# Optimization experiments

Hardware: AMD Instinct MI355X
Metric: run time of the kernel (lower is better)

Reference implementation:

```python
import jax, jax.numpy as jnp
import numpy as np

B, V, L, C, CA = 4, 16, 1024, 256, 256
MASK_VAL = 1e10  # original: triu(ones) * 10**10 subtracted pre-softmax


def setup_inputs() -> dict:
    key = jax.random.key(0)
    ks = jax.random.split(key, 10)
    s = 0.05  # keep logits in a sane range; math is init-independent
    return {
        "X": jax.random.normal(ks[0], (B, V, L, C), jnp.float32),
        "Qw": jax.random.normal(ks[1], (V, C, CA), jnp.float32) * s,
        "Kw": jax.random.normal(ks[2], (V, C, CA), jnp.float32) * s,
        "Vw": jax.random.normal(ks[3], (V, C, CA), jnp.float32) * s,
        "Qb": jax.random.normal(ks[4], (CA,), jnp.float32) * s,
        "Kb": jax.random.normal(ks[5], (CA,), jnp.float32) * s,
        "Vb": jax.random.normal(ks[6], (CA,), jnp.float32) * s,
        "gama": jax.random.normal(ks[7], (1,), jnp.float32),
        "fc_w": jax.random.normal(ks[8], (C, CA), jnp.float32) * s,
        "fc_b": jax.random.normal(ks[9], (C,), jnp.float32) * s,
    }


def reference(X, Qw, Kw, Vw, Qb, Kb, Vb, gama, fc_w, fc_b):
    # per-variable projections: [B,v,L,C] x [v,C,Ca] -> [B,v,L,Ca]
    Q = jnp.einsum('bvlc,vca->bvla', X, Qw) + Qb
    K = jnp.einsum('bvlc,vca->bvla', X, Kw) + Kb
    Vp = jnp.einsum('bvlc,vca->bvla', X, Vw) + Vb
    # causal mask subtraction (no 1/sqrt(d) scaling in the original)
    Lc = X.shape[2]
    mask = jnp.triu(jnp.ones((Lc, Lc), X.dtype), 1) * MASK_VAL
    scores = jnp.einsum('bvla,bvma->bvlm', Q, K) - mask  # [B,v,L,L]
    alpha = jax.nn.softmax(scores, axis=-1)
    Va = jnp.einsum('bvlm,bvma->bvla', alpha, Vp)        # [B,v,L,Ca]
    # gated fc + residual: X + gama * fc(Va)
    return X + (jnp.einsum('bvla,ca->bvlc', Va, fc_w) + fc_b) * gama
```

## Files before the change

kernel.cpp:

```cpp
#include <hip/hip_runtime.h>

typedef __bf16 bf16_8 __attribute__((ext_vector_type(8)));
typedef float f32x4 __attribute__((ext_vector_type(4)));

#define MFMA16(a, b, c) __builtin_amdgcn_mfma_f32_16x16x32_bf16(a, b, c, 0, 0, 0)


__device__ __forceinline__ void load_lds16(const char* g, char* l) {
  __builtin_amdgcn_global_load_lds(
      (const __attribute__((address_space(1))) unsigned int*)g,
      (__attribute__((address_space(3))) unsigned int*)l, 16, 0, 0);
}

__global__ __launch_bounds__(256) void prep_kernel(
    const float* __restrict__ Qw, const float* __restrict__ Kw,
    const float* __restrict__ Vw, const float* __restrict__ fcw,
    const float* __restrict__ X,
    __bf16* __restrict__ Wfq, __bf16* __restrict__ Wfk,
    __bf16* __restrict__ Wfv, __bf16* __restrict__ fcb,
    __bf16* __restrict__ Xb)
{
  const int bid = blockIdx.x, t = threadIdx.x;
  if (bid < 192) {
    __shared__ __bf16 lds[64][264];
    const int m = bid >> 2, cblk = bid & 3;
    const int wsel = m >> 4, v = m & 15;
    const float* src = (wsel == 0 ? Qw : wsel == 1 ? Kw : Vw) + (size_t)v * 65536;
    __bf16* dst = (wsel == 0 ? Wfq : wsel == 1 ? Wfk : Wfv) + (size_t)v * 65536;
    const int c0 = cblk * 64;
    const int cl = t >> 2, seg = t & 3;
#pragma unroll
    for (int i = 0; i < 16; ++i) {
      float4 f = *(const float4*)(src + (size_t)(c0 + cl) * 256 + seg * 64 + i * 4);
      lds[cl][seg * 64 + i * 4 + 0] = (__bf16)f.x;
      lds[cl][seg * 64 + i * 4 + 1] = (__bf16)f.y;
      lds[cl][seg * 64 + i * 4 + 2] = (__bf16)f.z;
      lds[cl][seg * 64 + i * 4 + 3] = (__bf16)f.w;
    }
    __syncthreads();
    const int nn = t >> 4, l16 = t & 15;
#pragma unroll
    for (int i = 0; i < 8; ++i) {
      bf16_8 vv;
#pragma unroll
      for (int j = 0; j < 8; ++j) vv[j] = lds[i * 8 + j][t];
      const int c = c0 + i * 8;
      const int ks = c >> 5, lg = (c & 31) >> 3;
      const int g = (ks * 16 + nn) * 64 + lg * 16 + l16;
      *(bf16_8*)(dst + (size_t)g * 8) = vv;
    }
  } else if (bid < 208) {
    const int g0 = (bid - 192) * 512 + t * 2;
#pragma unroll
    for (int h = 0; h < 2; ++h) {
      int g = g0 + h;
      int ks = g >> 10, n = (g >> 6) & 15, lane = g & 63;
      const float* src = fcw + (size_t)(n * 16 + (lane & 15)) * 256
                             + ks * 32 + (lane >> 4) * 8;
      float4 f0 = *(const float4*)(src);
      float4 f1 = *(const float4*)(src + 4);
      bf16_8 vv;
      vv[0] = (__bf16)f0.x; vv[1] = (__bf16)f0.y; vv[2] = (__bf16)f0.z; vv[3] = (__bf16)f0.w;
      vv[4] = (__bf16)f1.x; vv[5] = (__bf16)f1.y; vv[6] = (__bf16)f1.z; vv[7] = (__bf16)f1.w;
      *(bf16_8*)(fcb + (size_t)g * 8) = vv;
    }
  } else {
    const size_t base = (size_t)(bid - 208) * 8192 + t * 32;
#pragma unroll
    for (int h = 0; h < 4; ++h) {
      float4 f0 = *(const float4*)(X + base + h * 8);
      float4 f1 = *(const float4*)(X + base + h * 8 + 4);
      bf16_8 vv;
      vv[0] = (__bf16)f0.x; vv[1] = (__bf16)f0.y; vv[2] = (__bf16)f0.z; vv[3] = (__bf16)f0.w;
      vv[4] = (__bf16)f1.x; vv[5] = (__bf16)f1.y; vv[6] = (__bf16)f1.z; vv[7] = (__bf16)f1.w;
      *(bf16_8*)(Xb + base + h * 8) = vv;
    }
  }
}

__global__ __launch_bounds__(256, 2) void proj_kernel(
    const __bf16* __restrict__ Xb,
    const __bf16* __restrict__ Wfq, const __bf16* __restrict__ Wfk,
    const __bf16* __restrict__ Wfv,
    const float* __restrict__ Qb, const float* __restrict__ Kb,
    const float* __restrict__ Vb,
    __bf16* __restrict__ Qo, __bf16* __restrict__ Ko, __bf16* __restrict__ VTo,
    int bv0)
{
  extern __shared__ char psmem[];
  char* rpb = psmem + 65536;

  const int t = threadIdx.x;
  const int w = t >> 6, lane = t & 63;
  const int l16 = lane & 15, lg = lane >> 4;

  const int nwg = gridDim.x * gridDim.y;
  const int hw = blockIdx.x + gridDim.x * blockIdx.y;
  int bvl, r12;
  if (nwg % 96 == 0) {
    const int per = nwg >> 3;
    const int lid = (hw & 7) * per + (hw >> 3);
    bvl = lid / 12; r12 = lid - bvl * 12;
  } else { bvl = blockIdx.y; r12 = blockIdx.x; }
  const int z = r12 >> 2, nh = (r12 >> 1) & 1, rh = r12 & 1;
  const int bvg = bv0 + bvl, v = bvg & 15;

  const __bf16* Wf = (z == 0 ? Wfq : z == 1 ? Wfk : Wfv) + (size_t)v * 65536;
  const float* bias = (z == 0 ? Qb : z == 1 ? Kb : Vb) + nh * 128;

  bf16_8 bw0[8], bw1[8];
#pragma unroll
  for (int ks = 0; ks < 8; ++ks) {
    const int nnb = nh * 8 + w * 2;
    bw0[ks] = *(const bf16_8*)(Wf + ((size_t)(ks * 16 + nnb) * 64 + lane) * 8);
    bw1[ks] = *(const bf16_8*)(Wf + ((size_t)(ks * 16 + nnb + 1) * 64 + lane) * 8);
  }

  const char* xb = (const char*)(Xb + ((size_t)(bvg * 1024 + rh * 512)) * 256);
  auto stageX = [&](int it, int pb) {
    const char* src0 = xb + (size_t)it * 32768;
    char* dst0 = psmem + pb * 32768;
#pragma unroll
    for (int i = 0; i < 8; ++i) {
      int p = i * 256 + t, r = p >> 5, c16 = p & 31;
      load_lds16(src0 + r * 512 + ((c16 * 16) ^ ((r & 7) << 4)),
                 dst0 + (i * 256 + w * 64) * 16);
    }
  };

  stageX(0, 0);

  const float bn0 = bias[w * 32 + l16];
  const float bn1 = bias[w * 32 + 16 + l16];
  f32x4 zero = {0.f, 0.f, 0.f, 0.f};
  const int xsw = (l16 & 7) << 4;

  for (int it = 0; it < 8; ++it) {
    const int cur = it & 1;
    __builtin_amdgcn_s_barrier();
    if (it < 7) {
      stageX(it + 1, cur ^ 1);
      asm volatile("s_waitcnt vmcnt(8)" ::: "memory");
    } else {
      asm volatile("s_waitcnt vmcnt(0)" ::: "memory");
    }
    __builtin_amdgcn_s_barrier();

    f32x4 acc[4][2];
#pragma unroll
    for (int m = 0; m < 4; ++m) { acc[m][0] = zero; acc[m][1] = zero; }

    const char* xt = psmem + cur * 32768 + l16 * 512;
#pragma unroll
    for (int ks = 0; ks < 8; ++ks) {
      const int co = (ks * 64 + lg * 16) ^ xsw;
      bf16_8 af[4];
#pragma unroll
      for (int m = 0; m < 4; ++m)
        af[m] = *(const bf16_8*)(xt + m * 8192 + co);
#pragma unroll
      for (int m = 0; m < 4; ++m) {
        acc[m][0] = MFMA16(af[m], bw0[ks], acc[m][0]);
        acc[m][1] = MFMA16(af[m], bw1[ks], acc[m][1]);
      }
    }

    const int row0 = rh * 512 + it * 64;
#pragma unroll
    for (int n = 0; n < 2; ++n) {
      float bn = n ? bn1 : bn0;
      int col2 = (w * 32 + n * 16 + l16) * 2;
#pragma unroll
      for (int m = 0; m < 4; ++m)
#pragma unroll
        for (int j = 0; j < 4; ++j) {
          int r = m * 16 + lg * 4 + j;
          *(__bf16*)(rpb + r * 256 + (col2 ^ ((r & 7) << 4))) = (__bf16)(acc[m][n][j] + bn);
        }
    }
    asm volatile("s_waitcnt lgkmcnt(0)" ::: "memory");
    __builtin_amdgcn_s_barrier();

    if (z < 2) {
      __bf16* out = (z == 0 ? Qo : Ko) + (size_t)(bvl * 1024 + row0) * 256;
#pragma unroll
      for (int i = 0; i < 4; ++i) {
        int e = i * 256 + t, rr = e >> 4, cl = (e & 15) * 8;
        bf16_8 d = *(const bf16_8*)(rpb + rr * 256 + ((cl * 2) ^ ((rr & 7) << 4)));
        int gcol = (z == 1) ? (nh * 128 + (cl ^ ((rr & 7) * 8))) : (nh * 128 + cl);
        *(bf16_8*)(out + (size_t)rr * 256 + gcol) = d;
      }
    } else {
      const int kt = rh * 8 + it;
      const int cal = t >> 1, half = t & 1;
      __bf16* dst = VTo + (size_t)bvl * 262144 + (size_t)kt * 16384
                    + (size_t)(nh * 128 + cal) * 64;
#pragma unroll
      for (int i = 0; i < 4; ++i) {
        int q = half * 4 + i;
        int k0 = (q ^ (cal & 7)) * 8;
        bf16_8 vv;
#pragma unroll
        for (int j = 0; j < 8; ++j)
          vv[j] = *(const __bf16*)(rpb + (k0 + j) * 256 + ((cal * 2) ^ (j << 4)));
        *(bf16_8*)(dst + q * 8) = vv;
      }
    }
  }
}

__global__ __launch_bounds__(512, 2) void attn_kernel(
    const __bf16* __restrict__ Qg, const __bf16* __restrict__ Kg,
    const __bf16* __restrict__ VTg, const __bf16* __restrict__ Fc,
    const float* __restrict__ Xg, const float* __restrict__ fc_b,
    const float* __restrict__ gama, float* __restrict__ Out, int bv0)
{
  extern __shared__ char smem[];
  __bf16 (*Pt)[72] = (__bf16(*)[72])(smem + 131072);

  const int t = threadIdx.x;
  const int w = t >> 6, lane = t & 63;
  const int l16 = lane & 15, lg = lane >> 4;

  const int nwg = gridDim.x * gridDim.y;
  const int hw = blockIdx.x + gridDim.x * blockIdx.y;
  int bvl, qb;
  if (nwg == 512) {
    const int x = hw & 7, j = hw >> 3;
    bvl = x * 8 + ((j >> 5) << 2) + (j & 3);
    qb  = 7 - ((j >> 2) & 7);
  } else { bvl = blockIdx.x; qb = 7 - (int)blockIdx.y; }
  const int bvg = bv0 + bvl;
  const int ktmax = 2 * qb + 1;

  const char* Kb = (const char*)(Kg + (size_t)bvl * 262144);
  const char* Vb = (const char*)(VTg + (size_t)bvl * 262144);

  bf16_8 qf[8];
  const __bf16* qp = Qg + ((size_t)(bvl * 1024 + qb * 128 + w * 16 + l16)) * 256 + lg * 8;
#pragma unroll
  for (int ks = 0; ks < 8; ++ks) qf[ks] = *(const bf16_8*)(qp + ks * 32);

  f32x4 zero = {0.f, 0.f, 0.f, 0.f};
  f32x4 oacc[16];
#pragma unroll
  for (int n = 0; n < 16; ++n) oacc[n] = zero;
  float rs[4] = {0.f, 0.f, 0.f, 0.f};

  const int swz = (l16 & 7) << 4;
  const int p1 = (lg * 16) ^ (swz & 0x30);
  const int o_e = swz & 0x40;
  const int o_o = 64 ^ (swz & 0x40);

  auto stage = [&](int kt, int pb) {
    const char* kg = Kb + (size_t)kt * 32768;
    const char* vg = Vb + (size_t)kt * 32768;
    char* kl = smem + pb * 32768;
    char* vl = smem + 65536 + pb * 32768;
#pragma unroll
    for (int i = 0; i < 4; ++i) {
      int go = (i * 512 + t) * 16;
      int lo = (i * 512 + w * 64) * 16;
      load_lds16(kg + go, kl + lo);
      load_lds16(vg + go, vl + lo);
    }
  };

  stage(0, 0);

  for (int kt = 0; kt <= ktmax; ++kt) {
    const int cur = kt & 1;

    __builtin_amdgcn_s_barrier();
    if (kt < ktmax) {
      stage(kt + 1, cur ^ 1);
      asm volatile("s_waitcnt vmcnt(8)" ::: "memory");
    } else {
      asm volatile("s_waitcnt vmcnt(0)" ::: "memory");
    }
    __builtin_amdgcn_s_barrier();

    const bool skip = (kt * 64) > (qb * 128 + w * 16 + 15);
    if (!skip) {
      const char* krow = smem + cur * 32768 + l16 * 512 + p1;
      f32x4 sacc[4];
#pragma unroll
      for (int n = 0; n < 4; ++n) sacc[n] = zero;
      __builtin_amdgcn_s_setprio(1);
#pragma unroll
      for (int ks = 0; ks < 8; ++ks) {
        const int cb = (ks >> 1) * 128 + ((ks & 1) ? o_o : o_e);
#pragma unroll
        for (int n = 0; n < 4; ++n) {
          bf16_8 kb = *(const bf16_8*)(krow + n * 8192 + cb);
          sacc[n] = MFMA16(qf[ks], kb, sacc[n]);
        }
      }
      __builtin_amdgcn_s_setprio(0);

      const bool edge = (kt * 64 + 63) > (qb * 128 + w * 16);
      const int qrow = qb * 128 + w * 16 + lg * 4;
#pragma unroll
      for (int n = 0; n < 4; ++n) {
        int kglob = kt * 64 + n * 16 + l16;
#pragma unroll
        for (int j = 0; j < 4; ++j) {
          float p = __expf(sacc[n][j]);
          if (edge && kglob > qrow + j) p = 0.f;
          rs[j] += p;
          Pt[w * 16 + lg * 4 + j][n * 16 + l16] = (__bf16)p;
        }
      }
      asm volatile("s_waitcnt lgkmcnt(0)" ::: "memory");

      const char* vrow = smem + 65536 + cur * 32768 + l16 * 128 + p1;
      __builtin_amdgcn_s_setprio(1);
#pragma unroll
      for (int k2 = 0; k2 < 2; ++k2) {
        bf16_8 pa = *(const bf16_8*)&Pt[w * 16 + l16][k2 * 32 + lg * 8];
        const int cb = k2 ? o_o : o_e;
#pragma unroll
        for (int n = 0; n < 16; ++n) {
          bf16_8 vv = *(const bf16_8*)(vrow + n * 2048 + cb);
          oacc[n] = MFMA16(pa, vv, oacc[n]);
        }
      }
      __builtin_amdgcn_s_setprio(0);
    }
  }

  __syncthreads();

#pragma unroll
  for (int j = 0; j < 4; ++j) {
    float s = rs[j];
    s += __shfl_xor(s, 1); s += __shfl_xor(s, 2);
    s += __shfl_xor(s, 4); s += __shfl_xor(s, 8);
    rs[j] = 1.0f / s;
  }

  __bf16* Va = (__bf16*)smem;
#pragma unroll
  for (int n = 0; n < 16; ++n) {
#pragma unroll
    for (int j = 0; j < 4; ++j) {
      int r = w * 16 + lg * 4 + j;
      int c = n * 16 + l16;
      Va[r * 256 + (c ^ ((r & 7) * 8))] = (__bf16)(oacc[n][j] * rs[j]);
    }
  }
  __syncthreads();

  f32x4 facc[16];
#pragma unroll
  for (int n = 0; n < 16; ++n) facc[n] = zero;
#pragma unroll
  for (int ks = 0; ks < 8; ++ks) {
    int cc = (ks * 32 + lg * 8) ^ ((l16 & 7) * 8);
    bf16_8 pa = *(const bf16_8*)(Va + (w * 16 + l16) * 256 + cc);
    const __bf16* fp = Fc + (size_t)ks * 8192 + lane * 8;
#pragma unroll
    for (int n = 0; n < 16; ++n) {
      bf16_8 fb = *(const bf16_8*)(fp + n * 512);
      facc[n] = MFMA16(pa, fb, facc[n]);
    }
  }

  const float g = gama[0];
  const size_t base = ((size_t)(bvg * 1024 + qb * 128 + w * 16)) * 256;
#pragma unroll
  for (int n = 0; n < 16; ++n) {
    int col = n * 16 + l16;
    float fbc = fc_b[col];
#pragma unroll
    for (int j = 0; j < 4; ++j) {
      size_t idx = base + (size_t)(lg * 4 + j) * 256 + col;
      Out[idx] = Xg[idx] + (facc[n][j] + fbc) * g;
    }
  }
}

extern "C" void kernel_launch(void* const* d_in, const int* in_sizes, int n_in,
                              void* d_out, int out_size, void* d_ws, size_t ws_size,
                              hipStream_t stream) {
  const float* X    = (const float*)d_in[0];
  const float* Qw   = (const float*)d_in[1];
  const float* Kw   = (const float*)d_in[2];
  const float* Vw   = (const float*)d_in[3];
  const float* Qb   = (const float*)d_in[4];
  const float* Kb   = (const float*)d_in[5];
  const float* Vb   = (const float*)d_in[6];
  const float* gama = (const float*)d_in[7];
  const float* fcw  = (const float*)d_in[8];
  const float* fcb  = (const float*)d_in[9];
  float* out = (float*)d_out;

  char* ws = (char*)d_ws;
  const size_t wbytes = (size_t)(6u << 20) + (128u << 10) + (32u << 20);
  const size_t perbv  = 3ull * 1024 * 256 * 2;
  if (ws_size < wbytes + perbv) return;
  int chunk = (int)((ws_size - wbytes) / perbv);
  if (chunk > 64) chunk = 64;
  int nchunks = (64 + chunk - 1) / chunk;
  chunk = (64 + nchunks - 1) / nchunks;

  __bf16* Wfq = (__bf16*)(ws);
  __bf16* Wfk = (__bf16*)(ws + (2u << 20));
  __bf16* Wfv = (__bf16*)(ws + (4u << 20));
  __bf16* Fcb = (__bf16*)(ws + (6u << 20));
  __bf16* Xb  = (__bf16*)(ws + (6u << 20) + (128u << 10));
  __bf16* Qo  = (__bf16*)(ws + wbytes);
  __bf16* Ko  = Qo + (size_t)chunk * 262144;
  __bf16* VTo = Ko + (size_t)chunk * 262144;

  prep_kernel<<<2256, 256, 0, stream>>>(Qw, Kw, Vw, fcw, X, Wfq, Wfk, Wfv, Fcb, Xb);

  const int psmem = 2 * 32768 + 64 * 128 * 2;
  (void)hipFuncSetAttribute(reinterpret_cast<const void*>(proj_kernel),
                            hipFuncAttributeMaxDynamicSharedMemorySize, psmem);
  const int smem = 4 * 32768 + 128 * 72 * 2;
  (void)hipFuncSetAttribute(reinterpret_cast<const void*>(attn_kernel),
                            hipFuncAttributeMaxDynamicSharedMemorySize, smem);

  for (int bv0 = 0; bv0 < 64; bv0 += chunk) {
    int nb = 64 - bv0; if (nb > chunk) nb = chunk;
    proj_kernel<<<dim3(12, nb), 256, psmem, stream>>>(Xb, Wfq, Wfk, Wfv, Qb, Kb, Vb,
                                                      Qo, Ko, VTo, bv0);
    attn_kernel<<<dim3(nb, 8), 512, smem, stream>>>(Qo, Ko, VTo, Fcb, X, fcb, gama,
                                                    out, bv0);
  }
}
```

Measured before the change: 168.0 us.

## Pair causal query blocks per workgroup and give each wave two query tiles

Each workgroup now processes two 128-row query blocks, u and 7-u, so that causal work is balanced across workgroups, and the grid is halved. Each wave handles 32 query rows as two 16-row groups that share each K and V fragment loaded from LDS, doubling MFMA work per LDS read. The P staging buffer becomes a swizzled 256x128-byte layout. This raises register pressure, since accumulators double, and removes the previous XCD-aware block remapping.

```diff
diff --git a/kernel.cpp b/kernel.cpp
--- a/kernel.cpp
+++ b/kernel.cpp
@@ -216,36 +216,34 @@
     const float* __restrict__ gama, float* __restrict__ Out, int bv0)
 {
   extern __shared__ char smem[];
-  __bf16 (*Pt)[72] = (__bf16(*)[72])(smem + 131072);
+  char* ptb = smem + 131072;
 
   const int t = threadIdx.x;
   const int w = t >> 6, lane = t & 63;
   const int l16 = lane & 15, lg = lane >> 4;
-
-  const int nwg = gridDim.x * gridDim.y;
-  const int hw = blockIdx.x + gridDim.x * blockIdx.y;
-  int bvl, qb;
-  if (nwg == 512) {
-    const int x = hw & 7, j = hw >> 3;
-    bvl = x * 8 + ((j >> 5) << 2) + (j & 3);
-    qb  = 7 - ((j >> 2) & 7);
-  } else { bvl = blockIdx.x; qb = 7 - (int)blockIdx.y; }
-  const int bvg = bv0 + bvl;
-  const int ktmax = 2 * qb + 1;
+  const int bvl = blockIdx.x, bvg = bv0 + bvl;
+  const int u = (int)blockIdx.y;
+  const int q0w = (w < 4) ? (u * 128 + w * 32) : ((7 - u) * 128 + (w - 4) * 32);
+  const int ktmax = 15 - 2 * u;
 
   const char* Kb = (const char*)(Kg + (size_t)bvl * 262144);
   const char* Vb = (const char*)(VTg + (size_t)bvl * 262144);
 
-  bf16_8 qf[8];
-  const __bf16* qp = Qg + ((size_t)(bvl * 1024 + qb * 128 + w * 16 + l16)) * 256 + lg * 8;
-#pragma unroll
-  for (int ks = 0; ks < 8; ++ks) qf[ks] = *(const bf16_8*)(qp + ks * 32);
+  bf16_8 qf[2][8];
+#pragma unroll
+  for (int g = 0; g < 2; ++g) {
+    const __bf16* qp = Qg + ((size_t)(bvl * 1024 + q0w + g * 16 + l16)) * 256 + lg * 8;
+#pragma unroll
+    for (int ks = 0; ks < 8; ++ks) qf[g][ks] = *(const bf16_8*)(qp + ks * 32);
+  }
 
   f32x4 zero = {0.f, 0.f, 0.f, 0.f};
-  f32x4 oacc[16];
-#pragma unroll
-  for (int n = 0; n < 16; ++n) oacc[n] = zero;
-  float rs[4] = {0.f, 0.f, 0.f, 0.f};
+  f32x4 oacc[2][16];
+#pragma unroll
+  for (int g = 0; g < 2; ++g)
+#pragma unroll
+    for (int n = 0; n < 16; ++n) oacc[g][n] = zero;
+  float rs[2][4] = {{0.f, 0.f, 0.f, 0.f}, {0.f, 0.f, 0.f, 0.f}};
 
   const int swz = (l16 & 7) << 4;
   const int p1 = (lg * 16) ^ (swz & 0x30);
@@ -280,12 +278,12 @@
     }
     __builtin_amdgcn_s_barrier();
 
-    const bool skip = (kt * 64) > (qb * 128 + w * 16 + 15);
+    const bool skip = (kt * 64) > (q0w + 31);
     if (!skip) {
       const char* krow = smem + cur * 32768 + l16 * 512 + p1;
-      f32x4 sacc[4];
-#pragma unroll
-      for (int n = 0; n < 4; ++n) sacc[n] = zero;
+      f32x4 sacc[2][4];
+#pragma unroll
+      for (int n = 0; n < 4; ++n) { sacc[0][n] = zero; sacc[1][n] = zero; }
       __builtin_amdgcn_s_setprio(1);
 #pragma unroll
       for (int ks = 0; ks < 8; ++ks) {
@@ -293,36 +291,48 @@
 #pragma unroll
         for (int n = 0; n < 4; ++n) {
           bf16_8 kb = *(const bf16_8*)(krow + n * 8192 + cb);
-          sacc[n] = MFMA16(qf[ks], kb, sacc[n]);
+          sacc[0][n] = MFMA16(qf[0][ks], kb, sacc[0][n]);
+          sacc[1][n] = MFMA16(qf[1][ks], kb, sacc[1][n]);
         }
       }
       __builtin_amdgcn_s_setprio(0);
 
-      const bool edge = (kt * 64 + 63) > (qb * 128 + w * 16);
-      const int qrow = qb * 128 + w * 16 + lg * 4;
-#pragma unroll
-      for (int n = 0; n < 4; ++n) {
-        int kglob = kt * 64 + n * 16 + l16;
-#pragma unroll
-        for (int j = 0; j < 4; ++j) {
-          float p = __expf(sacc[n][j]);
-          if (edge && kglob > qrow + j) p = 0.f;
-          rs[j] += p;
-          Pt[w * 16 + lg * 4 + j][n * 16 + l16] = (__bf16)p;
+#pragma unroll
+      for (int g = 0; g < 2; ++g) {
+        const int q0g = q0w + g * 16;
+        const bool edge = (kt * 64 + 63) > q0g;
+        const int qrow = q0g + lg * 4;
+        const int rbase = w * 32 + g * 16 + lg * 4;
+#pragma unroll
+        for (int n = 0; n < 4; ++n) {
+          int kglob = kt * 64 + n * 16 + l16;
+          int c2 = (n * 16 + l16) * 2;
+#pragma unroll
+          for (int j = 0; j < 4; ++j) {
+            float p = __expf(sacc[g][n][j]);
+            if (edge && kglob > qrow + j) p = 0.f;
+            rs[g][j] += p;
+            int r = rbase + j;
+            *(__bf16*)(ptb + r * 128 + (c2 ^ ((r & 7) << 4))) = (__bf16)p;
+          }
         }
       }
       asm volatile("s_waitcnt lgkmcnt(0)" ::: "memory");
 
       const char* vrow = smem + 65536 + cur * 32768 + l16 * 128 + p1;
+      const int rr0 = w * 32 + l16;
       __builtin_amdgcn_s_setprio(1);
 #pragma unroll
       for (int k2 = 0; k2 < 2; ++k2) {
-        bf16_8 pa = *(const bf16_8*)&Pt[w * 16 + l16][k2 * 32 + lg * 8];
+        const int po = (k2 * 64 + lg * 16) ^ ((l16 & 7) << 4);
+        bf16_8 pa0 = *(const bf16_8*)(ptb + rr0 * 128 + po);
+        bf16_8 pa1 = *(const bf16_8*)(ptb + (rr0 + 16) * 128 + po);
         const int cb = k2 ? o_o : o_e;
 #pragma unroll
         for (int n = 0; n < 16; ++n) {
           bf16_8 vv = *(const bf16_8*)(vrow + n * 2048 + cb);
-          oacc[n] = MFMA16(pa, vv, oacc[n]);
+          oacc[0][n] = MFMA16(pa0, vv, oacc[0][n]);
+          oacc[1][n] = MFMA16(pa1, vv, oacc[1][n]);
         }
       }
       __builtin_amdgcn_s_setprio(0);
@@ -332,50 +342,62 @@
   __syncthreads();
 
 #pragma unroll
-  for (int j = 0; j < 4; ++j) {
-    float s = rs[j];
-    s += __shfl_xor(s, 1); s += __shfl_xor(s, 2);
-    s += __shfl_xor(s, 4); s += __shfl_xor(s, 8);
-    rs[j] = 1.0f / s;
-  }
-
-  __bf16* Va = (__bf16*)smem;
-#pragma unroll
-  for (int n = 0; n < 16; ++n) {
+  for (int g = 0; g < 2; ++g)
 #pragma unroll
     for (int j = 0; j < 4; ++j) {
-      int r = w * 16 + lg * 4 + j;
-      int c = n * 16 + l16;
-      Va[r * 256 + (c ^ ((r & 7) * 8))] = (__bf16)(oacc[n][j] * rs[j]);
-    }
-  }
+      float s = rs[g][j];
+      s += __shfl_xor(s, 1); s += __shfl_xor(s, 2);
+      s += __shfl_xor(s, 4); s += __shfl_xor(s, 8);
+      rs[g][j] = 1.0f / s;
+    }
+
+#pragma unroll
+  for (int g = 0; g < 2; ++g)
+#pragma unroll
+    for (int n = 0; n < 16; ++n) {
+      int c2 = (n * 16 + l16) * 2;
+#pragma unroll
+      for (int j = 0; j < 4; ++j) {
+        int r = w * 32 + g * 16 + lg * 4 + j;
+        *(__bf16*)(smem + r * 512 + (c2 ^ ((r & 7) << 4))) =
+            (__bf16)(oacc[g][n][j] * rs[g][j]);
+      }
+    }
   __syncthreads();
 
-  f32x4 facc[16];
-#pragma unroll
-  for (int n = 0; n < 16; ++n) facc[n] = zero;
+  f32x4 facc[2][16];
+#pragma unroll
+  for (int g = 0; g < 2; ++g)
+#pragma unroll
+    for (int n = 0; n < 16; ++n) facc[g][n] = zero;
+  const int rv0 = w * 32 + l16;
 #pragma unroll
   for (int ks = 0; ks < 8; ++ks) {
-    int cc = (ks * 32 + lg * 8) ^ ((l16 & 7) * 8);
-    bf16_8 pa = *(const bf16_8*)(Va + (w * 16 + l16) * 256 + cc);
+    const int po = (ks * 64 + lg * 16) ^ ((l16 & 7) << 4);
+    bf16_8 pa0 = *(const bf16_8*)(smem + rv0 * 512 + po);
+    bf16_8 pa1 = *(const bf16_8*)(smem + (rv0 + 16) * 512 + po);
     const __bf16* fp = Fc + (size_t)ks * 8192 + lane * 8;
 #pragma unroll
     for (int n = 0; n < 16; ++n) {
       bf16_8 fb = *(const bf16_8*)(fp + n * 512);
-      facc[n] = MFMA16(pa, fb, facc[n]);
-    }
-  }
-
-  const float g = gama[0];
-  const size_t base = ((size_t)(bvg * 1024 + qb * 128 + w * 16)) * 256;
-#pragma unroll
-  for (int n = 0; n < 16; ++n) {
-    int col = n * 16 + l16;
-    float fbc = fc_b[col];
-#pragma unroll
-    for (int j = 0; j < 4; ++j) {
-      size_t idx = base + (size_t)(lg * 4 + j) * 256 + col;
-      Out[idx] = Xg[idx] + (facc[n][j] + fbc) * g;
+      facc[0][n] = MFMA16(pa0, fb, facc[0][n]);
+      facc[1][n] = MFMA16(pa1, fb, facc[1][n]);
+    }
+  }
+
+  const float gm = gama[0];
+#pragma unroll
+  for (int g = 0; g < 2; ++g) {
+    const size_t base = ((size_t)(bvg * 1024 + q0w + g * 16)) * 256;
+#pragma unroll
+    for (int n = 0; n < 16; ++n) {
+      int col = n * 16 + l16;
+      float fbc = fc_b[col];
+#pragma unroll
+      for (int j = 0; j < 4; ++j) {
+        size_t idx = base + (size_t)(lg * 4 + j) * 256 + col;
+        Out[idx] = Xg[idx] + (facc[g][n][j] + fbc) * gm;
+      }
     }
   }
 }
@@ -418,7 +440,7 @@
   const int psmem = 2 * 32768 + 64 * 128 * 2;
   (void)hipFuncSetAttribute(reinterpret_cast<const void*>(proj_kernel),
                             hipFuncAttributeMaxDynamicSharedMemorySize, psmem);
-  const int smem = 4 * 32768 + 128 * 72 * 2;
+  const int smem = 4 * 32768 + 256 * 128;
   (void)hipFuncSetAttribute(reinterpret_cast<const void*>(attn_kernel),
                             hipFuncAttributeMaxDynamicSharedMemorySize, smem);
 
@@ -426,7 +448,7 @@
     int nb = 64 - bv0; if (nb > chunk) nb = chunk;
     proj_kernel<<<dim3(12, nb), 256, psmem, stream>>>(Xb, Wfq, Wfk, Wfv, Qb, Kb, Vb,
                                                       Qo, Ko, VTo, bv0);
-    attn_kernel<<<dim3(nb, 8), 512, smem, stream>>>(Qo, Ko, VTo, Fcb, X, fcb, gama,
+    attn_kernel<<<dim3(nb, 4), 512, smem, stream>>>(Qo, Ko, VTo, Fcb, X, fcb, gama,
                                                     out, bv0);
   }
 }
```

New measurement: 223.1 us. +32.8%, slower.

## Load V fragments directly from global in MFMA order, drop V LDS staging

Applied to the files above, without the earlier changes.

The projection kernel now writes V^T in a fragment-major layout, so each lane's MFMA B-operand is one contiguous 16-byte chunk. The attention kernel reads V straight from global/L2 in that order instead of staging it through double-buffered LDS. The P tile moves to an XOR-swizzled 128-byte-row layout. LDS use drops from about 146KB to 80KB and the async wait count is adjusted to match. In exchange, global-load latency now sits directly in front of the PV MFMAs with no prefetch, which may stall the inner loop.

```diff
diff --git a/kernel.cpp b/kernel.cpp
--- a/kernel.cpp
+++ b/kernel.cpp
@@ -192,18 +192,20 @@
       }
     } else {
       const int kt = rh * 8 + it;
-      const int cal = t >> 1, half = t & 1;
-      __bf16* dst = VTo + (size_t)bvl * 262144 + (size_t)kt * 16384
-                    + (size_t)(nh * 128 + cal) * 64;
+      const int lane6 = t & 63, gi = t >> 6;
+      __bf16* dstb = VTo + (size_t)bvl * 262144 + (size_t)kt * 16384;
 #pragma unroll
       for (int i = 0; i < 4; ++i) {
-        int q = half * 4 + i;
-        int k0 = (q ^ (cal & 7)) * 8;
+        int idx = gi * 4 + i;
+        int k2 = idx >> 3, nloc = idx & 7;
         bf16_8 vv;
 #pragma unroll
-        for (int j = 0; j < 8; ++j)
-          vv[j] = *(const __bf16*)(rpb + (k0 + j) * 256 + ((cal * 2) ^ (j << 4)));
-        *(bf16_8*)(dst + q * 8) = vv;
+        for (int j = 0; j < 8; ++j) {
+          int r = k2 * 32 + (lane6 >> 4) * 8 + j;
+          int cl = nloc * 16 + (lane6 & 15);
+          vv[j] = *(const __bf16*)(rpb + r * 256 + ((cl * 2) ^ ((r & 7) << 4)));
+        }
+        *(bf16_8*)(dstb + ((size_t)(k2 * 16 + nh * 8 + nloc) * 64 + lane6) * 8) = vv;
       }
     }
   }
@@ -216,7 +218,7 @@
     const float* __restrict__ gama, float* __restrict__ Out, int bv0)
 {
   extern __shared__ char smem[];
-  __bf16 (*Pt)[72] = (__bf16(*)[72])(smem + 131072);
+  char* ptb = smem + 65536;
 
   const int t = threadIdx.x;
   const int w = t >> 6, lane = t & 63;
@@ -234,7 +236,7 @@
   const int ktmax = 2 * qb + 1;
 
   const char* Kb = (const char*)(Kg + (size_t)bvl * 262144);
-  const char* Vb = (const char*)(VTg + (size_t)bvl * 262144);
+  const __bf16* Vf = VTg + (size_t)bvl * 262144;
 
   bf16_8 qf[8];
   const __bf16* qp = Qg + ((size_t)(bvl * 1024 + qb * 128 + w * 16 + l16)) * 256 + lg * 8;
@@ -254,15 +256,12 @@
 
   auto stage = [&](int kt, int pb) {
     const char* kg = Kb + (size_t)kt * 32768;
-    const char* vg = Vb + (size_t)kt * 32768;
     char* kl = smem + pb * 32768;
-    char* vl = smem + 65536 + pb * 32768;
 #pragma unroll
     for (int i = 0; i < 4; ++i) {
       int go = (i * 512 + t) * 16;
       int lo = (i * 512 + w * 64) * 16;
       load_lds16(kg + go, kl + lo);
-      load_lds16(vg + go, vl + lo);
     }
   };
 
@@ -274,7 +273,7 @@
     __builtin_amdgcn_s_barrier();
     if (kt < ktmax) {
       stage(kt + 1, cur ^ 1);
-      asm volatile("s_waitcnt vmcnt(8)" ::: "memory");
+      asm volatile("s_waitcnt vmcnt(4)" ::: "memory");
     } else {
       asm volatile("s_waitcnt vmcnt(0)" ::: "memory");
     }
@@ -303,25 +302,27 @@
 #pragma unroll
       for (int n = 0; n < 4; ++n) {
         int kglob = kt * 64 + n * 16 + l16;
+        int c2 = (n * 16 + l16) * 2;
 #pragma unroll
         for (int j = 0; j < 4; ++j) {
           float p = __expf(sacc[n][j]);
           if (edge && kglob > qrow + j) p = 0.f;
           rs[j] += p;
-          Pt[w * 16 + lg * 4 + j][n * 16 + l16] = (__bf16)p;
+          int r = w * 16 + lg * 4 + j;
+          *(__bf16*)(ptb + r * 128 + (c2 ^ ((r & 7) << 4))) = (__bf16)p;
         }
       }
       asm volatile("s_waitcnt lgkmcnt(0)" ::: "memory");
 
-      const char* vrow = smem + 65536 + cur * 32768 + l16 * 128 + p1;
+      const __bf16* vt = Vf + (size_t)kt * 16384;
+      const int prow = (w * 16 + l16) * 128;
       __builtin_amdgcn_s_setprio(1);
 #pragma unroll
       for (int k2 = 0; k2 < 2; ++k2) {
-        bf16_8 pa = *(const bf16_8*)&Pt[w * 16 + l16][k2 * 32 + lg * 8];
-        const int cb = k2 ? o_o : o_e;
+        bf16_8 pa = *(const bf16_8*)(ptb + prow + ((k2 * 64 + lg * 16) ^ ((l16 & 7) << 4)));
 #pragma unroll
         for (int n = 0; n < 16; ++n) {
-          bf16_8 vv = *(const bf16_8*)(vrow + n * 2048 + cb);
+          bf16_8 vv = *(const bf16_8*)(vt + ((size_t)(k2 * 16 + n) * 64 + lane) * 8);
           oacc[n] = MFMA16(pa, vv, oacc[n]);
         }
       }
@@ -418,7 +419,7 @@
   const int psmem = 2 * 32768 + 64 * 128 * 2;
   (void)hipFuncSetAttribute(reinterpret_cast<const void*>(proj_kernel),
                             hipFuncAttributeMaxDynamicSharedMemorySize, psmem);
-  const int smem = 4 * 32768 + 128 * 72 * 2;
+  const int smem = 2 * 32768 + 128 * 128;
   (void)hipFuncSetAttribute(reinterpret_cast<const void*>(attn_kernel),
                             hipFuncAttributeMaxDynamicSharedMemorySize, smem);
 
```

Measured after the change: 263.3 us. 56.7% more time.
